# Kernel tuning notes

Measured on AMD Instinct MI355X. Metric: run time of the kernel, lower is better.

Reference implementation:

```python
import jax, jax.numpy as jnp
import numpy as np

SHIFT = 1  # fixed realization of the random +/-1 shift_direction in __init__


def setup_inputs() -> dict:
    key = jax.random.key(0)
    k1, k2, k3 = jax.random.split(key, 3)
    x = jax.random.normal(k1, (1, 128, 56, 56), dtype=jnp.float32)
    w0 = jax.random.normal(k2, (32, 2, 3, 3), dtype=jnp.float32)   # weights[0]
    w1 = jax.random.normal(k3, (4, 64), dtype=jnp.float32)         # weights[1]
    return {"x": x, "w0": w0, "w1": w1}


def reference(x, w0, w1):
    # x: [1,128,56,56] -> [1,64,2,56,56]
    t3 = x.reshape(1, 64, 2, 56, 56)
    # 1x1 channel mix: contract the 64 axis with w1 [4,64]
    t4 = jnp.einsum('kjlmn,ij->kilmn', t3, w1)  # [1,4,2,56,56]
    # First unfold: kernel 3 along the last spatial axis (h2), zero pad 1.
    p1 = jnp.pad(t4, ((0, 0), (0, 0), (0, 0), (0, 0), (1, 1)))
    A = jnp.stack([p1[..., k:k + 56] for k in range(3)], axis=-2)  # [1,4,2,56,3,56]
    # Second unfold: kernel 3 along the SAME (already unfolded) position axis,
    # zero pad 1 applied to the unfolded tensor (matches torch's two-stage unfold).
    p2 = jnp.pad(A, ((0, 0), (0, 0), (0, 0), (0, 0), (0, 0), (1, 1)))
    B = jnp.stack([p2[..., k:k + 56] for k in range(3)], axis=-2)  # [1,4,2,56,3,3,56]
    # Contract group channel j=2 and both kernel offsets i,k with w0 [32,2,3,3]
    t6 = jnp.einsum('mpjoikn,ljik->mlpon', B, w0)  # [1,32,4,56,56]
    y = t6.reshape(1, 128, 56, 56)
    # Cyclic shift along H (axis 2)
    return jnp.roll(y, SHIFT, axis=2)
```

## Files before the change

### kernel.cpp

```cpp
#include <hip/hip_runtime.h>


__global__ __launch_bounds__(256) void fused_shift_unfold_kernel(
    const float* __restrict__ x,
    const float* __restrict__ w0,
    const float* __restrict__ w1,
    float* __restrict__ out)
{
    __shared__ float s_x[128 * 56];
    __shared__ float s_t4[8][58];
    __shared__ float s_w0[144];
    __shared__ float s_w1[256];

    const int tid = threadIdx.x;
    const int h   = blockIdx.x;
    const int by  = blockIdx.y;
    const int o   = (h + 55) % 56;

    s_w1[tid] = w1[tid];
    if (tid < 144) s_w0[tid] = w0[by * 144 + tid];
    if (tid < 8) { s_t4[tid][0] = 0.f; s_t4[tid][57] = 0.f; }

    const float* xrow = x + o * 56;
    for (int t = tid; t < 128 * 56; t += 256) {
        int ch = t / 56;
        int n  = t - ch * 56;
        s_x[t] = xrow[ch * 3136 + n];
    }
    __syncthreads();

    for (int v = tid; v < 448; v += 256) {
        int p  = v / 112;
        int r  = v - p * 112;
        int jg = r / 56;
        int n  = r - jg * 56;
        const float* wrow = &s_w1[p * 64];
        const float* xs   = &s_x[jg * 56 + n];
        float acc = 0.f;
        #pragma unroll
        for (int q = 0; q < 64; ++q)
            acc += wrow[q] * xs[q * 112];
        s_t4[p * 2 + jg][n + 1] = acc;
    }
    __syncthreads();

    float* orow = out + h * 56;
    for (int v = tid; v < 32 * 56; v += 256) {
        int cl = v / 56;
        int n  = v - cl * 56;
        int c  = by * 32 + cl;
        int ll = cl >> 2;
        int p  = c & 3;
        float acc = 0.f;
        #pragma unroll
        for (int jg = 0; jg < 2; ++jg) {
            const float* row = s_t4[p * 2 + jg];
            const float* wj  = &s_w0[(ll * 2 + jg) * 9];
            #pragma unroll
            for (int k = 0; k < 3; ++k) {
                int m = n + k - 1;
                if ((unsigned)m < 56u) {
                    acc += wj[0 * 3 + k] * row[m    ];
                    acc += wj[1 * 3 + k] * row[m + 1];
                    acc += wj[2 * 3 + k] * row[m + 2];
                }
            }
        }
        orow[c * 3136 + n] = acc;
    }
}

extern "C" void kernel_launch(void* const* d_in, const int* in_sizes, int n_in,
                              void* d_out, int out_size, void* d_ws, size_t ws_size,
                              hipStream_t stream) {
    (void)in_sizes; (void)n_in; (void)out_size; (void)d_ws; (void)ws_size;
    const float* x  = (const float*)d_in[0];
    const float* w0 = (const float*)d_in[1];
    const float* w1 = (const float*)d_in[2];
    float* out = (float*)d_out;

    dim3 grid(56, 4);
    fused_shift_unfold_kernel<<<grid, 256, 0, stream>>>(x, w0, w1, out);
}
```

Measured before the change: 63.73 us.

## Split blocks by channel-mix group p and drop redundant shared input staging

Each block now handles one group p of the 4-way channel mix for one output row. It computes only the 2x56 t4 values that group needs, reading x directly from global memory, instead of staging all 128 input channels of the row in shared memory and computing all 8 t4 rows. The four blocks per row used to each recompute the full channel mix. Now that work is split across them, and shared memory drops from about 30KB, which should raise occupancy. The cost is that each block loads all 576 w0 weights and the channel-mix loads become strided global reads with partial ILP.

```diff
diff --git a/kernel.cpp b/kernel.cpp
--- a/kernel.cpp
+++ b/kernel.cpp
@@ -7,66 +7,59 @@
     const float* __restrict__ w1,
     float* __restrict__ out)
 {
-    __shared__ float s_x[128 * 56];
-    __shared__ float s_t4[8][58];
-    __shared__ float s_w0[144];
-    __shared__ float s_w1[256];
+    __shared__ float s_t4[2][58];
+    __shared__ float s_w0[576];
 
     const int tid = threadIdx.x;
     const int h   = blockIdx.x;
-    const int by  = blockIdx.y;
+    const int p   = blockIdx.y;
     const int o   = (h + 55) % 56;
 
-    s_w1[tid] = w1[tid];
-    if (tid < 144) s_w0[tid] = w0[by * 144 + tid];
-    if (tid < 8) { s_t4[tid][0] = 0.f; s_t4[tid][57] = 0.f; }
-
-    const float* xrow = x + o * 56;
-    for (int t = tid; t < 128 * 56; t += 256) {
-        int ch = t / 56;
-        int n  = t - ch * 56;
-        s_x[t] = xrow[ch * 3136 + n];
-    }
-    __syncthreads();
-
-    for (int v = tid; v < 448; v += 256) {
-        int p  = v / 112;
-        int r  = v - p * 112;
-        int jg = r / 56;
-        int n  = r - jg * 56;
-        const float* wrow = &s_w1[p * 64];
-        const float* xs   = &s_x[jg * 56 + n];
-        float acc = 0.f;
+    if (tid < 112) {
+        const int j = (tid >= 56);
+        const int n = tid - j * 56;
+        const float* xp = x + j * 3136 + o * 56 + n;
+        const float* wp = w1 + p * 64;
+        float a0 = 0.f, a1 = 0.f, a2 = 0.f, a3 = 0.f;
         #pragma unroll
-        for (int q = 0; q < 64; ++q)
-            acc += wrow[q] * xs[q * 112];
-        s_t4[p * 2 + jg][n + 1] = acc;
+        for (int q = 0; q < 64; q += 4) {
+            a0 += wp[q + 0] * xp[(q + 0) * 6272];
+            a1 += wp[q + 1] * xp[(q + 1) * 6272];
+            a2 += wp[q + 2] * xp[(q + 2) * 6272];
+            a3 += wp[q + 3] * xp[(q + 3) * 6272];
+        }
+        s_t4[j][n + 1] = (a0 + a1) + (a2 + a3);
+    } else {
+        const int t = tid - 112;
+        #pragma unroll
+        for (int r = 0; r < 4; ++r)
+            s_w0[t * 4 + r] = w0[t * 4 + r];
+        if (t < 4) s_t4[t >> 1][(t & 1) * 57] = 0.f;
     }
     __syncthreads();
 
     float* orow = out + h * 56;
-    for (int v = tid; v < 32 * 56; v += 256) {
-        int cl = v / 56;
-        int n  = v - cl * 56;
-        int c  = by * 32 + cl;
-        int ll = cl >> 2;
-        int p  = c & 3;
+    #pragma unroll
+    for (int it = 0; it < 7; ++it) {
+        const int v = tid + it * 256;
+        const int l = v / 56;
+        const int n = v - l * 56;
         float acc = 0.f;
         #pragma unroll
-        for (int jg = 0; jg < 2; ++jg) {
-            const float* row = s_t4[p * 2 + jg];
-            const float* wj  = &s_w0[(ll * 2 + jg) * 9];
+        for (int j = 0; j < 2; ++j) {
+            const float* row = s_t4[j];
+            const float* wj  = &s_w0[(l * 2 + j) * 9];
             #pragma unroll
             for (int k = 0; k < 3; ++k) {
-                int m = n + k - 1;
+                const int m = n + k - 1;
                 if ((unsigned)m < 56u) {
-                    acc += wj[0 * 3 + k] * row[m    ];
-                    acc += wj[1 * 3 + k] * row[m + 1];
-                    acc += wj[2 * 3 + k] * row[m + 2];
+                    acc += wj[0 + k] * row[m    ];
+                    acc += wj[3 + k] * row[m + 1];
+                    acc += wj[6 + k] * row[m + 2];
                 }
             }
         }
-        orow[c * 3136 + n] = acc;
+        orow[(l * 4 + p) * 3136 + n] = acc;
     }
 }
 
```

New measurement: 61.89 us. -2.9%, faster.
